# Kernel tuning notes

Hardware: AMD Instinct MI355X
Metric: run time of the kernel (lower is better)

Reference implementation:

```python
import jax, jax.numpy as jnp
import numpy as np

N_NODES = 50000
N_EDGES = 500000
IN_CH = 128
HID = 32
HEADS = 4
OUT_CH = 64
NEG_SLOPE = 0.2


def setup_inputs() -> dict:
    key = jax.random.key(0)
    ks = jax.random.split(key, 12)
    s = 0.1  # weight init scale
    x = jax.random.normal(ks[0], (N_NODES, IN_CH), jnp.float32)
    edge_index = jax.random.randint(ks[1], (2, N_EDGES), 0, N_NODES)
    # conv1: GATv2Conv(IN_CH, HID, heads=HEADS)
    W1l = jax.random.normal(ks[2], (IN_CH, HEADS * HID), jnp.float32) * s  # lin_l (source)
    W1r = jax.random.normal(ks[3], (IN_CH, HEADS * HID), jnp.float32) * s  # lin_r (target)
    att1 = jax.random.normal(ks[4], (HEADS, HID), jnp.float32) * s
    b1 = jnp.zeros((HEADS * HID,), jnp.float32)
    # conv2: GATv2Conv(HEADS*HID, OUT_CH, heads=1, concat=False)
    W2l = jax.random.normal(ks[5], (HEADS * HID, OUT_CH), jnp.float32) * s
    W2r = jax.random.normal(ks[6], (HEADS * HID, OUT_CH), jnp.float32) * s
    att2 = jax.random.normal(ks[7], (1, OUT_CH), jnp.float32) * s
    b2 = jnp.zeros((OUT_CH,), jnp.float32)
    return {"x": x, "edge_index": edge_index, "W1l": W1l, "W1r": W1r,
            "att1": att1, "b1": b1, "W2l": W2l, "W2r": W2r, "att2": att2, "b2": b2}


def gatv2_conv(x, src, dst, Wl, Wr, att, heads, ch, num_nodes):
    """GATv2Conv message passing. Returns [N, heads, ch] (pre-bias, pre-concat)."""
    xl = (x @ Wl).reshape(num_nodes, heads, ch)  # source transform
    xr = (x @ Wr).reshape(num_nodes, heads, ch)  # target transform
    xl_e = xl[src]                               # [E, H, C] gathered source feats
    m = jax.nn.leaky_relu(xl_e + xr[dst], NEG_SLOPE)
    score = jnp.einsum('ehc,hc->eh', m, att)     # [E, H]
    # segment softmax over incoming edges per destination node
    smax = jax.ops.segment_max(score, dst, num_segments=num_nodes)
    smax = jnp.where(jnp.isfinite(smax), smax, 0.0)
    p = jnp.exp(score - smax[dst])
    denom = jax.ops.segment_sum(p, dst, num_segments=num_nodes)
    alpha = p / (denom[dst] + 1e-16)
    out = jax.ops.segment_sum(alpha[:, :, None] * xl_e, dst, num_segments=num_nodes)
    return out


def reference(x, edge_index, W1l, W1r, att1, b1, W2l, W2r, att2, b2):
    n = x.shape[0]
    loop = jnp.arange(n, dtype=edge_index.dtype)
    src = jnp.concatenate([edge_index[0], loop])  # add self-loops (PyG default)
    dst = jnp.concatenate([edge_index[1], loop])
    # dropout(p=0.6) is identity in eval mode
    h = gatv2_conv(x, src, dst, W1l, W1r, att1, HEADS, HID, n)
    h = h.reshape(n, HEADS * HID) + b1            # concat=True
    h = jax.nn.elu(h)
    o = gatv2_conv(h, src, dst, W2l, W2r, att2, 1, OUT_CH, n)  # [N, 1, OUT]
    o = o + b2                                     # concat=False, heads=1 -> mean == identity
    return o[:, 0, :]
```

## Files before the change

kernel.cpp:

```cpp
#include <hip/hip_runtime.h>
#include <hip/hip_bf16.h>
#include <math.h>

#define N_NODESC 50000
#define N_EDGESC 500000
#define E_TOT    (N_EDGESC + N_NODESC)
#define IN_CH 128
#define HID 32
#define HEADS 4
#define HC (HEADS*HID)
#define OUT_CH 64
#define NEG_SLOPE 0.2f
#define NB_SCAN 196
#define N_STRIPS (N_NODESC/16)
#define NB_HIST 2149
#define NB_PREP 24
#define NB_SPLIT 6250

typedef unsigned short u16;
typedef __attribute__((ext_vector_type(8))) short short8;
typedef __attribute__((ext_vector_type(8))) unsigned short ushort8v;
typedef __attribute__((ext_vector_type(4))) float floatx4;

__device__ __forceinline__ u16 f2bf(float f){
  unsigned u = __float_as_uint(f);
  return (u16)((u + 0x7FFFu + ((u >> 16) & 1u)) >> 16);
}
__device__ __forceinline__ float bf2f(u16 b){ return __uint_as_float(((unsigned)b) << 16); }
__device__ __forceinline__ float lrelu(float v){ return fmaxf(v, NEG_SLOPE*v); }

__device__ __forceinline__ void edge_sd(const int* __restrict__ ei, int e, int& s, int& d){
  if (e < N_EDGESC){ s = ei[e]; d = ei[N_EDGESC + e]; }
  else { s = e - N_EDGESC; d = s; }
}

__global__ void k_misc(const int* __restrict__ ei, int* __restrict__ deg,
                       const float* __restrict__ X, u16* __restrict__ xhi, u16* __restrict__ xlo,
                       const float* __restrict__ W1l, const float* __restrict__ W1r,
                       const float* __restrict__ W2l, const float* __restrict__ W2r,
                       u16* __restrict__ w1lh, u16* __restrict__ w1rh,
                       u16* __restrict__ w2lh, u16* __restrict__ w2rh){
  int b = blockIdx.x;
  if (b < NB_HIST){
    int e = b*256 + threadIdx.x;
    if (e < E_TOT){
      int s, d; edge_sd(ei, e, s, d);
      atomicAdd(&deg[d], 1);
    }
  } else if (b < NB_HIST + NB_PREP){
    int bb = b - NB_HIST;
    const float* W; u16 *Th; int N, base;
    if (bb < 8)      { W=W1l; Th=w1lh; N=HC;     base=bb;    }
    else if (bb < 16){ W=W1r; Th=w1rh; N=HC;     base=bb-8;  }
    else if (bb < 20){ W=W2l; Th=w2lh; N=OUT_CH; base=bb-16; }
    else             { W=W2r; Th=w2rh; N=OUT_CH; base=bb-20; }
    int tid = base*256 + threadIdx.x;
    int lane = tid & 63;
    int t = (tid >> 6) & 3;
    int c = tid >> 8;
    int k0 = t*32 + (lane>>4)*8;
    int n  = c*16 + (lane&15);
    #pragma unroll
    for (int j=0;j<8;j++){
      Th[(size_t)tid*8 + j] = f2bf(W[(size_t)(k0+j)*N + n]);
    }
  } else {
    int i = (b - NB_HIST - NB_PREP)*256 + threadIdx.x;
    if (i < N_NODESC*HC/4){
      float4 v = ((const float4*)X)[i];
      ushort4 h, l;
      h.x = f2bf(v.x); l.x = f2bf(v.x - bf2f(h.x));
      h.y = f2bf(v.y); l.y = f2bf(v.y - bf2f(h.y));
      h.z = f2bf(v.z); l.z = f2bf(v.z - bf2f(h.z));
      h.w = f2bf(v.w); l.w = f2bf(v.w - bf2f(h.w));
      ((ushort4*)xhi)[i] = h;
      ((ushort4*)xlo)[i] = l;
    }
  }
}

__global__ void k_scan_a(const int* __restrict__ deg, int* __restrict__ rs,
                         int* __restrict__ bsum){
  __shared__ int sh[256];
  int i = blockIdx.x*256 + threadIdx.x;
  int v = (i < N_NODESC) ? deg[i] : 0;
  sh[threadIdx.x] = v;
  __syncthreads();
  for (int off=1; off<256; off<<=1){
    int t = (threadIdx.x >= off) ? sh[threadIdx.x-off] : 0;
    __syncthreads();
    sh[threadIdx.x] += t;
    __syncthreads();
  }
  if (i < N_NODESC) rs[i] = sh[threadIdx.x] - v;
  if (threadIdx.x == 255) bsum[blockIdx.x] = sh[255];
}

__global__ void k_scan_bc(int* __restrict__ rs, const int* __restrict__ bsum,
                          int* __restrict__ cursor){
  __shared__ int sh[256];
  int v = (threadIdx.x < NB_SCAN) ? bsum[threadIdx.x] : 0;
  sh[threadIdx.x] = v;
  __syncthreads();
  for (int off=1; off<256; off<<=1){
    int t = (threadIdx.x >= off) ? sh[threadIdx.x-off] : 0;
    __syncthreads();
    sh[threadIdx.x] += t;
    __syncthreads();
  }
  int add = sh[blockIdx.x] - bsum[blockIdx.x];
  int i = blockIdx.x*256 + threadIdx.x;
  if (i < N_NODESC){
    int v2 = rs[i] + add;
    rs[i] = v2;
    cursor[i] = v2;
  }
}

__global__ void k_fill(const int* __restrict__ ei, int* __restrict__ cursor,
                       int* __restrict__ csrc){
  int e = blockIdx.x*blockDim.x + threadIdx.x;
  if (e >= E_TOT) return;
  int s, d; edge_sd(ei, e, s, d);
  int pos = atomicAdd(&cursor[d], 1);
  csrc[pos] = s;
}

template<int NCW, int SPB>
__launch_bounds__(256, 2)
__global__ void k_gemm_regB(const u16* __restrict__ Ahi, const u16* __restrict__ Alo,
                            const u16* __restrict__ BlT, const u16* __restrict__ BrT,
                            u16* __restrict__ Olb, u16* __restrict__ Orb){
  constexpr int NLD = 2*NCW*16;
  int wave = threadIdx.x >> 6, lane = threadIdx.x & 63;
  int m = lane & 15, quad = lane >> 4;
  bool isl = (wave < 2);
  int ctbase = (isl ? wave : wave - 2) * NCW;
  const u16* __restrict__ BT = isl ? BlT : BrT;
  u16* __restrict__ Ob = isl ? Olb : Orb;

  short8 breg[NCW][4];
  #pragma unroll
  for (int c=0;c<NCW;c++)
    #pragma unroll
    for (int t=0;t<4;t++)
      breg[c][t] = *(const short8*)(BT + ((size_t)(((ctbase+c)*4 + t)*64) + lane)*8);

  int strip0 = blockIdx.x * SPB;
  short8 ah[2][4], al[2][4];

  {
    const u16* p1 = Ahi + (size_t)(strip0*16 + m)*128 + quad*8;
    const u16* p2 = Alo + (size_t)(strip0*16 + m)*128 + quad*8;
    #pragma unroll
    for (int t=0;t<4;t++){
      ah[0][t] = *(const short8*)(p1 + t*32);
      al[0][t] = *(const short8*)(p2 + t*32);
    }
  }

  #pragma unroll
  for (int i=0;i<SPB;i++){
    int s = strip0 + i;
    if (s >= N_STRIPS) break;
    if (i+1 < SPB && s+1 < N_STRIPS){
      const u16* p1 = Ahi + (size_t)((s+1)*16 + m)*128 + quad*8;
      const u16* p2 = Alo + (size_t)((s+1)*16 + m)*128 + quad*8;
      #pragma unroll
      for (int t=0;t<4;t++){
        ah[(i+1)&1][t] = *(const short8*)(p1 + t*32);
        al[(i+1)&1][t] = *(const short8*)(p2 + t*32);
      }
    }
    const int b = i&1;
    floatx4 acc[NCW];
    #pragma unroll
    for (int c=0;c<NCW;c++) acc[c] = (floatx4){0.f,0.f,0.f,0.f};
    #pragma unroll
    for (int t=0;t<4;t++){
      #pragma unroll
      for (int c=0;c<NCW;c++){
        acc[c] = __builtin_amdgcn_mfma_f32_16x16x32_bf16(ah[b][t], breg[c][t], acc[c], 0,0,0);
        acc[c] = __builtin_amdgcn_mfma_f32_16x16x32_bf16(al[b][t], breg[c][t], acc[c], 0,0,0);
      }
    }
    int row0 = s*16;
    #pragma unroll
    for (int c=0;c<NCW;c++)
      #pragma unroll
      for (int r=0;r<4;r++)
        Ob[(size_t)(row0 + quad*4 + r)*NLD + (ctbase+c)*16 + m] = f2bf(acc[c][r]);
  }
}

__global__ void k_fused1(const int* __restrict__ rs, const int* __restrict__ deg,
                         const int* __restrict__ csrc, const u16* __restrict__ xlb,
                         const u16* __restrict__ xrb, const float* __restrict__ att,
                         const float* __restrict__ b1,
                         u16* __restrict__ Hhi, u16* __restrict__ Hlo){
  int wave = threadIdx.x >> 6;
  int lane = threadIdx.x & 63;
  int d = blockIdx.x*4 + wave;
  if (d >= N_NODESC) return;
  int g = lane >> 4;
  int l = lane & 15;

  float xrv[8], atv[8];
  {
    ushort8v xq = *(const ushort8v*)(xrb + (size_t)d*HC + 8*l);
    #pragma unroll
    for (int j=0;j<8;j++) xrv[j] = bf2f(xq[j]);
    float4 c = *(const float4*)(att + 8*l);
    float4 e = *(const float4*)(att + 8*l + 4);
    atv[0]=c.x; atv[1]=c.y; atv[2]=c.z; atv[3]=c.w;
    atv[4]=e.x; atv[5]=e.y; atv[6]=e.z; atv[7]=e.w;
  }

  int start = rs[d], degd = deg[d];

  float acc[8];
  #pragma unroll
  for (int j=0;j<8;j++) acc[j] = 0.f;
  float den = 0.f;

  int s_cur = csrc[start + ((g < degd) ? g : 0)];
  for (int i = 0; i < degd; i += 4){
    bool valid = (i + g < degd);
    int s = s_cur;
    int en = i + 4 + g;
    s_cur = csrc[start + ((en < degd) ? en : 0)];
    ushort8v q = *(const ushort8v*)(xlb + (size_t)s*HC + 8*l);
    float xv[8];
    float sc = 0.f;
    #pragma unroll
    for (int j=0;j<8;j++){
      xv[j] = bf2f(q[j]);
      sc = fmaf(lrelu(xv[j] + xrv[j]), atv[j], sc);
    }
    sc += __shfl_xor(sc, 1);
    sc += __shfl_xor(sc, 2);
    float p = valid ? __expf(sc) : 0.f;
    den += p;
    #pragma unroll
    for (int j=0;j<8;j++) acc[j] = fmaf(p, xv[j], acc[j]);
  }
  #pragma unroll
  for (int j=0;j<8;j++){
    acc[j] += __shfl_xor(acc[j], 16);
    acc[j] += __shfl_xor(acc[j], 32);
  }
  den += __shfl_xor(den, 16);
  den += __shfl_xor(den, 32);

  if (g == 0){
    float bv[8];
    float4 a = *(const float4*)(b1 + 8*l);
    float4 b = *(const float4*)(b1 + 8*l + 4);
    bv[0]=a.x; bv[1]=a.y; bv[2]=a.z; bv[3]=a.w;
    bv[4]=b.x; bv[5]=b.y; bv[6]=b.z; bv[7]=b.w;
    float inv = 1.f / (den + 1e-16f);
    u16 ohv[8], olv[8];
    #pragma unroll
    for (int j=0;j<8;j++){
      float o = acc[j]*inv + bv[j];
      o = (o > 0.f) ? o : (__expf(o) - 1.f);
      u16 h = f2bf(o);
      ohv[j] = h;
      olv[j] = f2bf(o - bf2f(h));
    }
    ushort4 h0 = {ohv[0],ohv[1],ohv[2],ohv[3]}, h1 = {ohv[4],ohv[5],ohv[6],ohv[7]};
    ushort4 l0 = {olv[0],olv[1],olv[2],olv[3]}, l1 = {olv[4],olv[5],olv[6],olv[7]};
    *(ushort4*)(Hhi + (size_t)d*HC + 8*l)     = h0;
    *(ushort4*)(Hhi + (size_t)d*HC + 8*l + 4) = h1;
    *(ushort4*)(Hlo + (size_t)d*HC + 8*l)     = l0;
    *(ushort4*)(Hlo + (size_t)d*HC + 8*l + 4) = l1;
  }
}

__global__ void k_fused2(const int* __restrict__ rs, const int* __restrict__ deg,
                         const int* __restrict__ csrc, const u16* __restrict__ xlb,
                         const u16* __restrict__ xrb, const float* __restrict__ att,
                         const float* __restrict__ b2, float* __restrict__ out){
  int wave = threadIdx.x >> 6;
  int lane = threadIdx.x & 63;
  int d = blockIdx.x*4 + wave;
  if (d >= N_NODESC) return;
  int g = lane >> 3;
  int l = lane & 7;

  float xrv[8], atv[8];
  {
    ushort8v xq = *(const ushort8v*)(xrb + (size_t)d*OUT_CH + 8*l);
    #pragma unroll
    for (int j=0;j<8;j++) xrv[j] = bf2f(xq[j]);
    float4 c = *(const float4*)(att + 8*l);
    float4 e = *(const float4*)(att + 8*l + 4);
    atv[0]=c.x; atv[1]=c.y; atv[2]=c.z; atv[3]=c.w;
    atv[4]=e.x; atv[5]=e.y; atv[6]=e.z; atv[7]=e.w;
  }

  int start = rs[d], degd = deg[d];

  float acc[8];
  #pragma unroll
  for (int j=0;j<8;j++) acc[j] = 0.f;
  float den = 0.f;

  int s_cur = csrc[start + ((g < degd) ? g : 0)];
  for (int i = 0; i < degd; i += 8){
    bool valid = (i + g < degd);
    int s = s_cur;
    int en = i + 8 + g;
    s_cur = csrc[start + ((en < degd) ? en : 0)];
    ushort8v q = *(const ushort8v*)(xlb + (size_t)s*OUT_CH + 8*l);
    float xv[8];
    float sc = 0.f;
    #pragma unroll
    for (int j=0;j<8;j++){
      xv[j] = bf2f(q[j]);
      sc = fmaf(lrelu(xv[j] + xrv[j]), atv[j], sc);
    }
    sc += __shfl_xor(sc, 1);
    sc += __shfl_xor(sc, 2);
    sc += __shfl_xor(sc, 4);
    float p = valid ? __expf(sc) : 0.f;
    den += p;
    #pragma unroll
    for (int j=0;j<8;j++) acc[j] = fmaf(p, xv[j], acc[j]);
  }
  #pragma unroll
  for (int j=0;j<8;j++){
    acc[j] += __shfl_xor(acc[j], 8);
    acc[j] += __shfl_xor(acc[j], 16);
    acc[j] += __shfl_xor(acc[j], 32);
  }
  den += __shfl_xor(den, 8);
  den += __shfl_xor(den, 16);
  den += __shfl_xor(den, 32);

  if (g == 0){
    float bv[8];
    float4 a = *(const float4*)(b2 + 8*l);
    float4 b = *(const float4*)(b2 + 8*l + 4);
    bv[0]=a.x; bv[1]=a.y; bv[2]=a.z; bv[3]=a.w;
    bv[4]=b.x; bv[5]=b.y; bv[6]=b.z; bv[7]=b.w;
    float inv = 1.f / (den + 1e-16f);
    float4 o0, o1;
    o0.x = acc[0]*inv + bv[0]; o0.y = acc[1]*inv + bv[1];
    o0.z = acc[2]*inv + bv[2]; o0.w = acc[3]*inv + bv[3];
    o1.x = acc[4]*inv + bv[4]; o1.y = acc[5]*inv + bv[5];
    o1.z = acc[6]*inv + bv[6]; o1.w = acc[7]*inv + bv[7];
    *(float4*)(out + (size_t)d*OUT_CH + 8*l)     = o0;
    *(float4*)(out + (size_t)d*OUT_CH + 8*l + 4) = o1;
  }
}

extern "C" void kernel_launch(void* const* d_in, const int* in_sizes, int n_in,
                              void* d_out, int out_size, void* d_ws, size_t ws_size,
                              hipStream_t stream) {
  const float* x    = (const float*)d_in[0];
  const int*   ei   = (const int*)d_in[1];
  const float* W1l  = (const float*)d_in[2];
  const float* W1r  = (const float*)d_in[3];
  const float* att1 = (const float*)d_in[4];
  const float* b1   = (const float*)d_in[5];
  const float* W2l  = (const float*)d_in[6];
  const float* W2r  = (const float*)d_in[7];
  const float* att2 = (const float*)d_in[8];
  const float* b2   = (const float*)d_in[9];
  float* out = (float*)d_out;

  float* ws = (float*)d_ws;
  size_t off = 0;
  u16* xl1b = (u16*)(ws + off); off += (size_t)N_NODESC*HC/2;
  u16* xr1b = (u16*)(ws + off); off += (size_t)N_NODESC*HC/2;
  u16* xl2b = (u16*)(ws + off); off += (size_t)N_NODESC*OUT_CH/2;
  u16* xr2b = (u16*)(ws + off); off += (size_t)N_NODESC*OUT_CH/2;
  u16* xhi = (u16*)(ws + off); off += (size_t)N_NODESC*HC/2;
  u16* xlo = (u16*)(ws + off); off += (size_t)N_NODESC*HC/2;
  u16* hhi = (u16*)(ws + off); off += (size_t)N_NODESC*HC/2;
  u16* hlo = (u16*)(ws + off); off += (size_t)N_NODESC*HC/2;
  u16* w1lh = (u16*)(ws + off); off += IN_CH*HC/2;
  u16* w1rh = (u16*)(ws + off); off += IN_CH*HC/2;
  u16* w2lh = (u16*)(ws + off); off += HC*OUT_CH/2;
  u16* w2rh = (u16*)(ws + off); off += HC*OUT_CH/2;
  int* deg    = (int*)(ws + off); off += N_NODESC;
  int* rs     = (int*)(ws + off); off += N_NODESC;
  int* cursor = (int*)(ws + off); off += N_NODESC;
  int* bsum   = (int*)(ws + off); off += 256;
  int* csrc   = (int*)(ws + off); off += E_TOT;

  hipMemsetAsync(deg, 0, N_NODESC*sizeof(int), stream);
  k_misc<<<NB_HIST + NB_PREP + NB_SPLIT, 256, 0, stream>>>(
      ei, deg, x, xhi, xlo, W1l, W1r, W2l, W2r, w1lh, w1rh, w2lh, w2rh);
  k_scan_a<<<NB_SCAN, 256, 0, stream>>>(deg, rs, bsum);
  k_scan_bc<<<NB_SCAN, 256, 0, stream>>>(rs, bsum, cursor);
  k_fill<<<(E_TOT+255)/256, 256, 0, stream>>>(ei, cursor, csrc);

  const int NB_G = (N_STRIPS + 3)/4;
  k_gemm_regB<4,4><<<NB_G, 256, 0, stream>>>(xhi, xlo, w1lh, w1rh, xl1b, xr1b);
  k_fused1<<<(N_NODESC+3)/4, 256, 0, stream>>>(rs, deg, csrc, xl1b, xr1b, att1, b1, hhi, hlo);

  k_gemm_regB<2,4><<<NB_G, 256, 0, stream>>>(hhi, hlo, w2lh, w2rh, xl2b, xr2b);
  k_fused2<<<(N_NODESC+3)/4, 256, 0, stream>>>(rs, deg, csrc, xl2b, xr2b, att2, b2, out);
}
```

Before: 250.1 us.

## Drop split-bf16 lo terms in GEMMs and batch neighbor index loads via shuffle

The hi/lo bf16 split of the activations (x and h) is removed, so each GEMM runs a single bf16 MFMA per tile and the lo buffers are no longer written or read. This halves the activation traffic and MFMA count, at the cost of lower accuracy in the linear transforms. The aggregation kernels also load up to 64 neighbor indices per wave in one coalesced read and hand them out with __shfl. This replaces the per-iteration serial csrc prefetch chain.

```diff
diff --git a/kernel.cpp b/kernel.cpp
--- a/kernel.cpp
+++ b/kernel.cpp
@@ -35,7 +35,7 @@
 }
 
 __global__ void k_misc(const int* __restrict__ ei, int* __restrict__ deg,
-                       const float* __restrict__ X, u16* __restrict__ xhi, u16* __restrict__ xlo,
+                       const float* __restrict__ X, u16* __restrict__ xhb,
                        const float* __restrict__ W1l, const float* __restrict__ W1r,
                        const float* __restrict__ W2l, const float* __restrict__ W2r,
                        u16* __restrict__ w1lh, u16* __restrict__ w1rh,
@@ -68,13 +68,9 @@
     int i = (b - NB_HIST - NB_PREP)*256 + threadIdx.x;
     if (i < N_NODESC*HC/4){
       float4 v = ((const float4*)X)[i];
-      ushort4 h, l;
-      h.x = f2bf(v.x); l.x = f2bf(v.x - bf2f(h.x));
-      h.y = f2bf(v.y); l.y = f2bf(v.y - bf2f(h.y));
-      h.z = f2bf(v.z); l.z = f2bf(v.z - bf2f(h.z));
-      h.w = f2bf(v.w); l.w = f2bf(v.w - bf2f(h.w));
-      ((ushort4*)xhi)[i] = h;
-      ((ushort4*)xlo)[i] = l;
+      ushort4 h;
+      h.x = f2bf(v.x); h.y = f2bf(v.y); h.z = f2bf(v.z); h.w = f2bf(v.w);
+      ((ushort4*)xhb)[i] = h;
     }
   }
 }
@@ -128,7 +124,7 @@
 
 template<int NCW, int SPB>
 __launch_bounds__(256, 2)
-__global__ void k_gemm_regB(const u16* __restrict__ Ahi, const u16* __restrict__ Alo,
+__global__ void k_gemm_regB(const u16* __restrict__ Ab,
                             const u16* __restrict__ BlT, const u16* __restrict__ BrT,
                             u16* __restrict__ Olb, u16* __restrict__ Orb){
   constexpr int NLD = 2*NCW*16;
@@ -147,16 +143,12 @@
       breg[c][t] = *(const short8*)(BT + ((size_t)(((ctbase+c)*4 + t)*64) + lane)*8);
 
   int strip0 = blockIdx.x * SPB;
-  short8 ah[2][4], al[2][4];
+  short8 ah[2][4];
 
   {
-    const u16* p1 = Ahi + (size_t)(strip0*16 + m)*128 + quad*8;
-    const u16* p2 = Alo + (size_t)(strip0*16 + m)*128 + quad*8;
-    #pragma unroll
-    for (int t=0;t<4;t++){
-      ah[0][t] = *(const short8*)(p1 + t*32);
-      al[0][t] = *(const short8*)(p2 + t*32);
-    }
+    const u16* p1 = Ab + (size_t)(strip0*16 + m)*128 + quad*8;
+    #pragma unroll
+    for (int t=0;t<4;t++) ah[0][t] = *(const short8*)(p1 + t*32);
   }
 
   #pragma unroll
@@ -164,13 +156,9 @@
     int s = strip0 + i;
     if (s >= N_STRIPS) break;
     if (i+1 < SPB && s+1 < N_STRIPS){
-      const u16* p1 = Ahi + (size_t)((s+1)*16 + m)*128 + quad*8;
-      const u16* p2 = Alo + (size_t)((s+1)*16 + m)*128 + quad*8;
-      #pragma unroll
-      for (int t=0;t<4;t++){
-        ah[(i+1)&1][t] = *(const short8*)(p1 + t*32);
-        al[(i+1)&1][t] = *(const short8*)(p2 + t*32);
-      }
+      const u16* p1 = Ab + (size_t)((s+1)*16 + m)*128 + quad*8;
+      #pragma unroll
+      for (int t=0;t<4;t++) ah[(i+1)&1][t] = *(const short8*)(p1 + t*32);
     }
     const int b = i&1;
     floatx4 acc[NCW];
@@ -179,10 +167,8 @@
     #pragma unroll
     for (int t=0;t<4;t++){
       #pragma unroll
-      for (int c=0;c<NCW;c++){
+      for (int c=0;c<NCW;c++)
         acc[c] = __builtin_amdgcn_mfma_f32_16x16x32_bf16(ah[b][t], breg[c][t], acc[c], 0,0,0);
-        acc[c] = __builtin_amdgcn_mfma_f32_16x16x32_bf16(al[b][t], breg[c][t], acc[c], 0,0,0);
-      }
     }
     int row0 = s*16;
     #pragma unroll
@@ -196,8 +182,7 @@
 __global__ void k_fused1(const int* __restrict__ rs, const int* __restrict__ deg,
                          const int* __restrict__ csrc, const u16* __restrict__ xlb,
                          const u16* __restrict__ xrb, const float* __restrict__ att,
-                         const float* __restrict__ b1,
-                         u16* __restrict__ Hhi, u16* __restrict__ Hlo){
+                         const float* __restrict__ b1, u16* __restrict__ Hb){
   int wave = threadIdx.x >> 6;
   int lane = threadIdx.x & 63;
   int d = blockIdx.x*4 + wave;
@@ -223,26 +208,27 @@
   for (int j=0;j<8;j++) acc[j] = 0.f;
   float den = 0.f;
 
-  int s_cur = csrc[start + ((g < degd) ? g : 0)];
-  for (int i = 0; i < degd; i += 4){
-    bool valid = (i + g < degd);
-    int s = s_cur;
-    int en = i + 4 + g;
-    s_cur = csrc[start + ((en < degd) ? en : 0)];
-    ushort8v q = *(const ushort8v*)(xlb + (size_t)s*HC + 8*l);
-    float xv[8];
-    float sc = 0.f;
-    #pragma unroll
-    for (int j=0;j<8;j++){
-      xv[j] = bf2f(q[j]);
-      sc = fmaf(lrelu(xv[j] + xrv[j]), atv[j], sc);
-    }
-    sc += __shfl_xor(sc, 1);
-    sc += __shfl_xor(sc, 2);
-    float p = valid ? __expf(sc) : 0.f;
-    den += p;
-    #pragma unroll
-    for (int j=0;j<8;j++) acc[j] = fmaf(p, xv[j], acc[j]);
+  for (int base = 0; base < degd; base += 64){
+    int nb = degd - base; if (nb > 64) nb = 64;
+    int idx = csrc[start + base + ((lane < nb) ? lane : 0)];
+    for (int i = 0; i < nb; i += 4){
+      bool valid = (i + g < nb);
+      int s = __shfl(idx, i + g);
+      ushort8v q = *(const ushort8v*)(xlb + (size_t)s*HC + 8*l);
+      float xv[8];
+      float sc = 0.f;
+      #pragma unroll
+      for (int j=0;j<8;j++){
+        xv[j] = bf2f(q[j]);
+        sc = fmaf(lrelu(xv[j] + xrv[j]), atv[j], sc);
+      }
+      sc += __shfl_xor(sc, 1);
+      sc += __shfl_xor(sc, 2);
+      float p = valid ? __expf(sc) : 0.f;
+      den += p;
+      #pragma unroll
+      for (int j=0;j<8;j++) acc[j] = fmaf(p, xv[j], acc[j]);
+    }
   }
   #pragma unroll
   for (int j=0;j<8;j++){
@@ -259,21 +245,16 @@
     bv[0]=a.x; bv[1]=a.y; bv[2]=a.z; bv[3]=a.w;
     bv[4]=b.x; bv[5]=b.y; bv[6]=b.z; bv[7]=b.w;
     float inv = 1.f / (den + 1e-16f);
-    u16 ohv[8], olv[8];
+    u16 ohv[8];
     #pragma unroll
     for (int j=0;j<8;j++){
       float o = acc[j]*inv + bv[j];
       o = (o > 0.f) ? o : (__expf(o) - 1.f);
-      u16 h = f2bf(o);
-      ohv[j] = h;
-      olv[j] = f2bf(o - bf2f(h));
+      ohv[j] = f2bf(o);
     }
     ushort4 h0 = {ohv[0],ohv[1],ohv[2],ohv[3]}, h1 = {ohv[4],ohv[5],ohv[6],ohv[7]};
-    ushort4 l0 = {olv[0],olv[1],olv[2],olv[3]}, l1 = {olv[4],olv[5],olv[6],olv[7]};
-    *(ushort4*)(Hhi + (size_t)d*HC + 8*l)     = h0;
-    *(ushort4*)(Hhi + (size_t)d*HC + 8*l + 4) = h1;
-    *(ushort4*)(Hlo + (size_t)d*HC + 8*l)     = l0;
-    *(ushort4*)(Hlo + (size_t)d*HC + 8*l + 4) = l1;
+    *(ushort4*)(Hb + (size_t)d*HC + 8*l)     = h0;
+    *(ushort4*)(Hb + (size_t)d*HC + 8*l + 4) = h1;
   }
 }
 
@@ -306,27 +287,28 @@
   for (int j=0;j<8;j++) acc[j] = 0.f;
   float den = 0.f;
 
-  int s_cur = csrc[start + ((g < degd) ? g : 0)];
-  for (int i = 0; i < degd; i += 8){
-    bool valid = (i + g < degd);
-    int s = s_cur;
-    int en = i + 8 + g;
-    s_cur = csrc[start + ((en < degd) ? en : 0)];
-    ushort8v q = *(const ushort8v*)(xlb + (size_t)s*OUT_CH + 8*l);
-    float xv[8];
-    float sc = 0.f;
-    #pragma unroll
-    for (int j=0;j<8;j++){
-      xv[j] = bf2f(q[j]);
-      sc = fmaf(lrelu(xv[j] + xrv[j]), atv[j], sc);
-    }
-    sc += __shfl_xor(sc, 1);
-    sc += __shfl_xor(sc, 2);
-    sc += __shfl_xor(sc, 4);
-    float p = valid ? __expf(sc) : 0.f;
-    den += p;
-    #pragma unroll
-    for (int j=0;j<8;j++) acc[j] = fmaf(p, xv[j], acc[j]);
+  for (int base = 0; base < degd; base += 64){
+    int nb = degd - base; if (nb > 64) nb = 64;
+    int idx = csrc[start + base + ((lane < nb) ? lane : 0)];
+    for (int i = 0; i < nb; i += 8){
+      bool valid = (i + g < nb);
+      int s = __shfl(idx, i + g);
+      ushort8v q = *(const ushort8v*)(xlb + (size_t)s*OUT_CH + 8*l);
+      float xv[8];
+      float sc = 0.f;
+      #pragma unroll
+      for (int j=0;j<8;j++){
+        xv[j] = bf2f(q[j]);
+        sc = fmaf(lrelu(xv[j] + xrv[j]), atv[j], sc);
+      }
+      sc += __shfl_xor(sc, 1);
+      sc += __shfl_xor(sc, 2);
+      sc += __shfl_xor(sc, 4);
+      float p = valid ? __expf(sc) : 0.f;
+      den += p;
+      #pragma unroll
+      for (int j=0;j<8;j++) acc[j] = fmaf(p, xv[j], acc[j]);
+    }
   }
   #pragma unroll
   for (int j=0;j<8;j++){
@@ -376,10 +358,8 @@
   u16* xr1b = (u16*)(ws + off); off += (size_t)N_NODESC*HC/2;
   u16* xl2b = (u16*)(ws + off); off += (size_t)N_NODESC*OUT_CH/2;
   u16* xr2b = (u16*)(ws + off); off += (size_t)N_NODESC*OUT_CH/2;
-  u16* xhi = (u16*)(ws + off); off += (size_t)N_NODESC*HC/2;
-  u16* xlo = (u16*)(ws + off); off += (size_t)N_NODESC*HC/2;
-  u16* hhi = (u16*)(ws + off); off += (size_t)N_NODESC*HC/2;
-  u16* hlo = (u16*)(ws + off); off += (size_t)N_NODESC*HC/2;
+  u16* xhb  = (u16*)(ws + off); off += (size_t)N_NODESC*HC/2;
+  u16* hb   = (u16*)(ws + off); off += (size_t)N_NODESC*HC/2;
   u16* w1lh = (u16*)(ws + off); off += IN_CH*HC/2;
   u16* w1rh = (u16*)(ws + off); off += IN_CH*HC/2;
   u16* w2lh = (u16*)(ws + off); off += HC*OUT_CH/2;
@@ -392,15 +372,15 @@
 
   hipMemsetAsync(deg, 0, N_NODESC*sizeof(int), stream);
   k_misc<<<NB_HIST + NB_PREP + NB_SPLIT, 256, 0, stream>>>(
-      ei, deg, x, xhi, xlo, W1l, W1r, W2l, W2r, w1lh, w1rh, w2lh, w2rh);
+      ei, deg, x, xhb, W1l, W1r, W2l, W2r, w1lh, w1rh, w2lh, w2rh);
   k_scan_a<<<NB_SCAN, 256, 0, stream>>>(deg, rs, bsum);
   k_scan_bc<<<NB_SCAN, 256, 0, stream>>>(rs, bsum, cursor);
   k_fill<<<(E_TOT+255)/256, 256, 0, stream>>>(ei, cursor, csrc);
 
   const int NB_G = (N_STRIPS + 3)/4;
-  k_gemm_regB<4,4><<<NB_G, 256, 0, stream>>>(xhi, xlo, w1lh, w1rh, xl1b, xr1b);
-  k_fused1<<<(N_NODESC+3)/4, 256, 0, stream>>>(rs, deg, csrc, xl1b, xr1b, att1, b1, hhi, hlo);
-
-  k_gemm_regB<2,4><<<NB_G, 256, 0, stream>>>(hhi, hlo, w2lh, w2rh, xl2b, xr2b);
+  k_gemm_regB<4,4><<<NB_G, 256, 0, stream>>>(xhb, w1lh, w1rh, xl1b, xr1b);
+  k_fused1<<<(N_NODESC+3)/4, 256, 0, stream>>>(rs, deg, csrc, xl1b, xr1b, att1, b1, hb);
+
+  k_gemm_regB<2,4><<<NB_G, 256, 0, stream>>>(hb, w2lh, w2rh, xl2b, xr2b);
   k_fused2<<<(N_NODESC+3)/4, 256, 0, stream>>>(rs, deg, csrc, xl2b, xr2b, att2, b2, out);
 }
```

New measurement: 230.4 us (median of 2 runs). 1.09x faster.
